# Performance work log

Hardware: AMD Instinct MI355X
Metric: run time of the kernel (lower is better)

Reference implementation:

```python
import jax, jax.numpy as jnp
import numpy as np

T = 8192
D_IN = 512
D_QK = 64
D_V = 64


def setup_inputs() -> dict:
    key = jax.random.key(0)
    kx, kq, kk, kv, kl = jax.random.split(key, 5)
    x = jax.random.normal(kx, (T, D_IN), dtype=jnp.float32)
    Wq = jax.random.normal(kq, (D_IN, D_QK), dtype=jnp.float32) * 0.02
    Wk = jax.random.normal(kk, (D_IN, D_QK), dtype=jnp.float32) * 0.02
    Wv = jax.random.normal(kv, (D_IN, D_V), dtype=jnp.float32) * 0.02
    l = jax.random.normal(kl, (T, T), dtype=jnp.float32) * 0.02
    return {"x": x, "Wq": Wq, "Wk": Wk, "Wv": Wv, "l": l}


def reference(x, Wq, Wk, Wv, l):
    # q: [T, d_qk], k: [T, d_qk], v: [T, d_v]
    q = x @ Wq
    k = x @ Wk
    v = x @ Wv
    # scores: [T, S] = (q k^T) elementwise-weighted by learned tril matrix
    scores = jnp.einsum("tn,sn->ts", q, k) * jnp.tril(l)
    # output: [T, d_v]
    return scores @ v
```

## Files before the change

### kernel.cpp

```cpp
#include <hip/hip_runtime.h>
#include <hip/hip_bf16.h>

#define TT 8192
#define DIN 512
#define DQK 64

typedef __attribute__((ext_vector_type(8))) short short8;
typedef __attribute__((ext_vector_type(4))) float f32x4;

__global__ __launch_bounds__(256) void init_kernel(
    const float* __restrict__ Wq, const float* __restrict__ Wk, const float* __restrict__ Wv,
    __hip_bfloat16* __restrict__ wtb, float* __restrict__ out, int n4)
{
    __shared__ float tile[64][65];
    const int b = blockIdx.x;
    const int tid = threadIdx.x;

    if (b >= 24) {
        const int nthr = 24 * 256;
        for (int i = (b - 24) * 256 + tid; i < n4; i += nthr)
            ((f32x4*)out)[i] = (f32x4){0.f, 0.f, 0.f, 0.f};
        return;
    }

    const int m = b >> 3;
    const float* W = m == 0 ? Wq : (m == 1 ? Wk : Wv);
    const int k0 = (b & 7) * 64;

    {
        const int col4 = (tid & 15) * 4;
        #pragma unroll
        for (int it = 0; it < 4; ++it) {
            const int row = (tid >> 4) + it * 16;
            float4 v = *(const float4*)&W[(size_t)(k0 + row) * DQK + col4];
            tile[row][col4 + 0] = v.x; tile[row][col4 + 1] = v.y;
            tile[row][col4 + 2] = v.z; tile[row][col4 + 3] = v.w;
        }
    }
    __syncthreads();
    {
        const int d = tid >> 2;
        const int kc = (tid & 3) * 16;
        short tmp[16];
        #pragma unroll
        for (int j = 0; j < 16; ++j) {
            __hip_bfloat16 h = __float2bfloat16(tile[kc + j][d]);
            tmp[j] = *(short*)&h;
        }
        short* dst = (short*)wtb + ((size_t)m * 64 + d) * DIN + k0 + kc;
        *(short8*)dst       = *(short8*)&tmp[0];
        *(short8*)(dst + 8) = *(short8*)&tmp[8];
    }
}

#define PP 72

__global__ __launch_bounds__(256) void proj_kernel(
    const float* __restrict__ x,
    const __hip_bfloat16* __restrict__ wtb,
    __hip_bfloat16* __restrict__ qb, __hip_bfloat16* __restrict__ kb,
    __hip_bfloat16* __restrict__ vt)
{
    __shared__ short xb[64][PP];
    __shared__ short wb[3][64][PP];

    const int rowBase = blockIdx.x * 64;
    const int tid = threadIdx.x;
    const int lane = tid & 63;
    const int w = tid >> 6;
    const int lo = lane & 15, hi = lane >> 4;

    f32x4 acc[3][4];
    #pragma unroll
    for (int m = 0; m < 3; ++m)
        #pragma unroll
        for (int cf = 0; cf < 4; ++cf) acc[m][cf] = (f32x4){0.f, 0.f, 0.f, 0.f};

    for (int kk = 0; kk < DIN; kk += 64) {
        {
            const int r = tid >> 2;
            const int c0 = (tid & 3) * 16;
            const float* xp = x + (size_t)(rowBase + r) * DIN + kk + c0;
            short tmp[16];
            #pragma unroll
            for (int j = 0; j < 16; j += 4) {
                float4 v = *(const float4*)(xp + j);
                __hip_bfloat16 h0 = __float2bfloat16(v.x);
                __hip_bfloat16 h1 = __float2bfloat16(v.y);
                __hip_bfloat16 h2 = __float2bfloat16(v.z);
                __hip_bfloat16 h3 = __float2bfloat16(v.w);
                tmp[j + 0] = *(short*)&h0; tmp[j + 1] = *(short*)&h1;
                tmp[j + 2] = *(short*)&h2; tmp[j + 3] = *(short*)&h3;
            }
            *(short8*)&xb[r][c0]     = *(short8*)&tmp[0];
            *(short8*)&xb[r][c0 + 8] = *(short8*)&tmp[8];
        }
        {
            const int d = tid >> 2;
            const int kc = (tid & 3) * 16;
            #pragma unroll
            for (int m = 0; m < 3; ++m) {
                const short* src = (const short*)wtb + ((size_t)m * 64 + d) * DIN + kk + kc;
                *(short8*)&wb[m][d][kc]     = *(const short8*)src;
                *(short8*)&wb[m][d][kc + 8] = *(const short8*)(src + 8);
            }
        }
        __syncthreads();

        short8 a0 = *(short8*)&xb[w * 16 + lo][hi * 8];
        short8 a1 = *(short8*)&xb[w * 16 + lo][32 + hi * 8];
        #pragma unroll
        for (int m = 0; m < 3; ++m) {
            #pragma unroll
            for (int cf = 0; cf < 4; ++cf) {
                short8 b0 = *(short8*)&wb[m][cf * 16 + lo][hi * 8];
                short8 b1 = *(short8*)&wb[m][cf * 16 + lo][32 + hi * 8];
                acc[m][cf] = __builtin_amdgcn_mfma_f32_16x16x32_bf16(a0, b0, acc[m][cf], 0, 0, 0);
                acc[m][cf] = __builtin_amdgcn_mfma_f32_16x16x32_bf16(a1, b1, acc[m][cf], 0, 0, 0);
            }
        }
        __syncthreads();
    }

    #pragma unroll
    for (int cf = 0; cf < 4; ++cf) {
        #pragma unroll
        for (int r = 0; r < 4; ++r) {
            const int tg = rowBase + w * 16 + hi * 4 + r;
            const int d  = cf * 16 + lo;
            __hip_bfloat16 hq = __float2bfloat16(acc[0][cf][r]);
            __hip_bfloat16 hk = __float2bfloat16(acc[1][cf][r]);
            __hip_bfloat16 hv = __float2bfloat16(acc[2][cf][r]);
            qb[(size_t)tg * DQK + d] = hq;
            kb[(size_t)tg * DQK + d] = hk;
            vt[(size_t)d * TT + tg]  = hv;
        }
    }
}

#define TM 128
#define TS 64
#define SCHUNK 512
#define LP 72

__global__ __launch_bounds__(512) void attn_kernel(
    const __hip_bfloat16* __restrict__ qb,
    const __hip_bfloat16* __restrict__ kb,
    const __hip_bfloat16* __restrict__ vt,
    const float* __restrict__ l,
    float* __restrict__ out)
{
    __shared__ short K_lds[TS][LP];
    __shared__ short V_lds[DQK][LP];
    __shared__ short S_lds[8][16][LP];

    const int bx = (gridDim.x - 1) - blockIdx.x;
    const int t0 = bx * TM;
    const int sStart = blockIdx.y * SCHUNK;
    if (sStart >= t0 + TM) return;
    const int sEnd = min(sStart + SCHUNK, t0 + TM);

    const int tid = threadIdx.x;
    const int lane = tid & 63;
    const int w = tid >> 6;
    const int lo = lane & 15, hi = lane >> 4;
    const int trow = t0 + w * 16;
    const int r0 = hi * 4;
    const bool waveActive = (sStart <= trow + 15);

    short8 qf0, qf1;
    {
        const short* qp = (const short*)qb + (size_t)(trow + lo) * DQK;
        qf0 = *(const short8*)(qp + hi * 8);
        qf1 = *(const short8*)(qp + 32 + hi * 8);
    }

    f32x4 acc_o[4];
    #pragma unroll
    for (int i = 0; i < 4; ++i) acc_o[i] = (f32x4){0.f, 0.f, 0.f, 0.f};

    float lvC[4][4];
    float lvN[4][4];
    if (waveActive) {
        #pragma unroll
        for (int sub = 0; sub < 4; ++sub) {
            const int s_glob = sStart + sub * 16 + lo;
            #pragma unroll
            for (int r = 0; r < 4; ++r) {
                const int tg = trow + r0 + r;
                lvC[sub][r] = (s_glob <= tg)
                    ? __builtin_nontemporal_load(&l[(size_t)tg * TT + s_glob]) : 0.f;
            }
        }
    }

    for (int s0 = sStart; s0 < sEnd; s0 += TS) {
        {
            const int row = tid >> 3;
            const int c8 = (tid & 7) * 8;
            *(short8*)&K_lds[row][c8] =
                *(const short8*)((const short*)kb + (size_t)(s0 + row) * DQK + c8);
            *(short8*)&V_lds[row][c8] =
                *(const short8*)((const short*)vt + (size_t)row * TT + s0 + c8);
        }
        __syncthreads();

        const bool active = (s0 <= trow + 15);
        const int sN = s0 + TS;
        const bool act_next = (sN < sEnd) && (sN <= trow + 15);

        if (act_next) {
            if (sN + 63 <= trow) {
                #pragma unroll
                for (int sub = 0; sub < 4; ++sub) {
                    const int s_glob = sN + sub * 16 + lo;
                    #pragma unroll
                    for (int r = 0; r < 4; ++r)
                        lvN[sub][r] = __builtin_nontemporal_load(
                            &l[(size_t)(trow + r0 + r) * TT + s_glob]);
                }
            } else {
                #pragma unroll
                for (int sub = 0; sub < 4; ++sub) {
                    const int s_glob = sN + sub * 16 + lo;
                    #pragma unroll
                    for (int r = 0; r < 4; ++r) {
                        const int tg = trow + r0 + r;
                        lvN[sub][r] = (s_glob <= tg)
                            ? __builtin_nontemporal_load(&l[(size_t)tg * TT + s_glob]) : 0.f;
                    }
                }
            }
        }

        if (active) {
            #pragma unroll
            for (int sub = 0; sub < 4; ++sub) {
                f32x4 acc = (f32x4){0.f, 0.f, 0.f, 0.f};
                short8 b0 = *(short8*)&K_lds[sub * 16 + lo][hi * 8];
                short8 b1 = *(short8*)&K_lds[sub * 16 + lo][32 + hi * 8];
                acc = __builtin_amdgcn_mfma_f32_16x16x32_bf16(qf0, b0, acc, 0, 0, 0);
                acc = __builtin_amdgcn_mfma_f32_16x16x32_bf16(qf1, b1, acc, 0, 0, 0);
                #pragma unroll
                for (int r = 0; r < 4; ++r) {
                    float sv = acc[r] * lvC[sub][r];
                    __hip_bfloat16 h = __float2bfloat16(sv);
                    S_lds[w][r0 + r][sub * 16 + lo] = *(short*)&h;
                }
            }
            short8 a0 = *(short8*)&S_lds[w][lo][hi * 8];
            short8 a1 = *(short8*)&S_lds[w][lo][32 + hi * 8];
            #pragma unroll
            for (int ds = 0; ds < 4; ++ds) {
                short8 b0 = *(short8*)&V_lds[ds * 16 + lo][hi * 8];
                short8 b1 = *(short8*)&V_lds[ds * 16 + lo][32 + hi * 8];
                acc_o[ds] = __builtin_amdgcn_mfma_f32_16x16x32_bf16(a0, b0, acc_o[ds], 0, 0, 0);
                acc_o[ds] = __builtin_amdgcn_mfma_f32_16x16x32_bf16(a1, b1, acc_o[ds], 0, 0, 0);
            }
        }
        __syncthreads();

        #pragma unroll
        for (int sub = 0; sub < 4; ++sub)
            #pragma unroll
            for (int r = 0; r < 4; ++r)
                lvC[sub][r] = lvN[sub][r];
    }

    if (waveActive) {
        #pragma unroll
        for (int ds = 0; ds < 4; ++ds) {
            #pragma unroll
            for (int r = 0; r < 4; ++r) {
                const int tg = trow + r0 + r;
                atomicAdd(&out[(size_t)tg * DQK + ds * 16 + lo], acc_o[ds][r]);
            }
        }
    }
}

extern "C" void kernel_launch(void* const* d_in, const int* in_sizes, int n_in,
                              void* d_out, int out_size, void* d_ws, size_t ws_size,
                              hipStream_t stream) {
    const float* x  = (const float*)d_in[0];
    const float* Wq = (const float*)d_in[1];
    const float* Wk = (const float*)d_in[2];
    const float* Wv = (const float*)d_in[3];
    const float* l  = (const float*)d_in[4];
    float* out = (float*)d_out;

    __hip_bfloat16* qb  = (__hip_bfloat16*)d_ws;
    __hip_bfloat16* kb  = qb + (size_t)TT * DQK;
    __hip_bfloat16* vt  = kb + (size_t)TT * DQK;
    __hip_bfloat16* wtb = vt + (size_t)TT * DQK;

    init_kernel<<<48, 256, 0, stream>>>(Wq, Wk, Wv, wtb, out, out_size / 4);
    proj_kernel<<<TT / 64, 256, 0, stream>>>(x, wtb, qb, kb, vt);
    attn_kernel<<<dim3(TT / TM, TT / SCHUNK), 512, 0, stream>>>(qb, kb, vt, l, out);
}
```

Before: 84.96 us.

## Transpose score MFMA to load l as float4 rows and pack S stores

```diff
diff --git a/kernel.cpp b/kernel.cpp
--- a/kernel.cpp
+++ b/kernel.cpp
@@ -7,6 +7,12 @@
 
 typedef __attribute__((ext_vector_type(8))) short short8;
 typedef __attribute__((ext_vector_type(4))) float f32x4;
+
+static __device__ __forceinline__ unsigned pack_bf16(float a, float b) {
+    __hip_bfloat16 ha = __float2bfloat16(a);
+    __hip_bfloat16 hb = __float2bfloat16(b);
+    return (unsigned)(*(unsigned short*)&ha) | ((unsigned)(*(unsigned short*)&hb) << 16);
+}
 
 __global__ __launch_bounds__(256) void init_kernel(
     const float* __restrict__ Wq, const float* __restrict__ Wk, const float* __restrict__ Wv,
@@ -140,7 +146,7 @@
 
 #define TM 128
 #define TS 64
-#define SCHUNK 512
+#define SCHUNK 256
 #define LP 72
 
 __global__ __launch_bounds__(512) void attn_kernel(
@@ -154,8 +160,7 @@
     __shared__ short V_lds[DQK][LP];
     __shared__ short S_lds[8][16][LP];
 
-    const int bx = (gridDim.x - 1) - blockIdx.x;
-    const int t0 = bx * TM;
+    const int t0 = blockIdx.x * TM;
     const int sStart = blockIdx.y * SCHUNK;
     if (sStart >= t0 + TM) return;
     const int sEnd = min(sStart + SCHUNK, t0 + TM);
@@ -165,12 +170,12 @@
     const int w = tid >> 6;
     const int lo = lane & 15, hi = lane >> 4;
     const int trow = t0 + w * 16;
-    const int r0 = hi * 4;
+    const int tmine = trow + lo;
     const bool waveActive = (sStart <= trow + 15);
 
     short8 qf0, qf1;
     {
-        const short* qp = (const short*)qb + (size_t)(trow + lo) * DQK;
+        const short* qp = (const short*)qb + (size_t)tmine * DQK;
         qf0 = *(const short8*)(qp + hi * 8);
         qf1 = *(const short8*)(qp + 32 + hi * 8);
     }
@@ -179,17 +184,22 @@
     #pragma unroll
     for (int i = 0; i < 4; ++i) acc_o[i] = (f32x4){0.f, 0.f, 0.f, 0.f};
 
-    float lvC[4][4];
-    float lvN[4][4];
+    const float* lrow = l + (size_t)tmine * TT;
+    const int sb = 4 * hi;
+
+    f32x4 lvC[4];
+    f32x4 lvN[4];
     if (waveActive) {
         #pragma unroll
         for (int sub = 0; sub < 4; ++sub) {
-            const int s_glob = sStart + sub * 16 + lo;
-            #pragma unroll
-            for (int r = 0; r < 4; ++r) {
-                const int tg = trow + r0 + r;
-                lvC[sub][r] = (s_glob <= tg)
-                    ? __builtin_nontemporal_load(&l[(size_t)tg * TT + s_glob]) : 0.f;
+            f32x4 raw = __builtin_nontemporal_load(
+                (const f32x4*)(lrow + sStart + sub * 16 + sb));
+            if (sStart + 63 <= trow) {
+                lvC[sub] = raw;
+            } else {
+                #pragma unroll
+                for (int r = 0; r < 4; ++r)
+                    lvC[sub][r] = (sStart + sub * 16 + sb + r <= tmine) ? raw[r] : 0.f;
             }
         }
     }
@@ -212,23 +222,17 @@
         if (act_next) {
             if (sN + 63 <= trow) {
                 #pragma unroll
-                for (int sub = 0; sub < 4; ++sub) {
-                    const int s_glob = sN + sub * 16 + lo;
-                    #pragma unroll
-                    for (int r = 0; r < 4; ++r)
-                        lvN[sub][r] = __builtin_nontemporal_load(
-                            &l[(size_t)(trow + r0 + r) * TT + s_glob]);
-                }
+                for (int sub = 0; sub < 4; ++sub)
+                    lvN[sub] = __builtin_nontemporal_load(
+                        (const f32x4*)(lrow + sN + sub * 16 + sb));
             } else {
                 #pragma unroll
                 for (int sub = 0; sub < 4; ++sub) {
-                    const int s_glob = sN + sub * 16 + lo;
+                    f32x4 raw = __builtin_nontemporal_load(
+                        (const f32x4*)(lrow + sN + sub * 16 + sb));
                     #pragma unroll
-                    for (int r = 0; r < 4; ++r) {
-                        const int tg = trow + r0 + r;
-                        lvN[sub][r] = (s_glob <= tg)
-                            ? __builtin_nontemporal_load(&l[(size_t)tg * TT + s_glob]) : 0.f;
-                    }
+                    for (int r = 0; r < 4; ++r)
+                        lvN[sub][r] = (sN + sub * 16 + sb + r <= tmine) ? raw[r] : 0.f;
                 }
             }
         }
@@ -239,14 +243,13 @@
                 f32x4 acc = (f32x4){0.f, 0.f, 0.f, 0.f};
                 short8 b0 = *(short8*)&K_lds[sub * 16 + lo][hi * 8];
                 short8 b1 = *(short8*)&K_lds[sub * 16 + lo][32 + hi * 8];
-                acc = __builtin_amdgcn_mfma_f32_16x16x32_bf16(qf0, b0, acc, 0, 0, 0);
-                acc = __builtin_amdgcn_mfma_f32_16x16x32_bf16(qf1, b1, acc, 0, 0, 0);
-                #pragma unroll
-                for (int r = 0; r < 4; ++r) {
-                    float sv = acc[r] * lvC[sub][r];
-                    __hip_bfloat16 h = __float2bfloat16(sv);
-                    S_lds[w][r0 + r][sub * 16 + lo] = *(short*)&h;
-                }
+                acc = __builtin_amdgcn_mfma_f32_16x16x32_bf16(b0, qf0, acc, 0, 0, 0);
+                acc = __builtin_amdgcn_mfma_f32_16x16x32_bf16(b1, qf1, acc, 0, 0, 0);
+                unsigned d0 = pack_bf16(acc[0] * lvC[sub][0], acc[1] * lvC[sub][1]);
+                unsigned d1 = pack_bf16(acc[2] * lvC[sub][2], acc[3] * lvC[sub][3]);
+                unsigned long long v = (unsigned long long)d0 |
+                                       ((unsigned long long)d1 << 32);
+                *(unsigned long long*)&S_lds[w][lo][sub * 16 + sb] = v;
             }
             short8 a0 = *(short8*)&S_lds[w][lo][hi * 8];
             short8 a1 = *(short8*)&S_lds[w][lo][32 + hi * 8];
@@ -262,9 +265,7 @@
 
         #pragma unroll
         for (int sub = 0; sub < 4; ++sub)
-            #pragma unroll
-            for (int r = 0; r < 4; ++r)
-                lvC[sub][r] = lvN[sub][r];
+            lvC[sub] = lvN[sub];
     }
 
     if (waveActive) {
@@ -272,7 +273,7 @@
         for (int ds = 0; ds < 4; ++ds) {
             #pragma unroll
             for (int r = 0; r < 4; ++r) {
-                const int tg = trow + r0 + r;
+                const int tg = trow + 4 * hi + r;
                 atomicAdd(&out[(size_t)tg * DQK + ds * 16 + lo], acc_o[ds][r]);
             }
         }
```

Measured after the change: 79.13 us. 1.07x faster.

## Split projection waves per matrix, halve attention S-chunk, drop reversed block order

Applied to the files above, without the earlier changes.

```diff
diff --git a/kernel.cpp b/kernel.cpp
--- a/kernel.cpp
+++ b/kernel.cpp
@@ -7,6 +7,16 @@
 
 typedef __attribute__((ext_vector_type(8))) short short8;
 typedef __attribute__((ext_vector_type(4))) float f32x4;
+
+static __device__ __forceinline__ short8 cvt8(const float* p) {
+    short tmp[8];
+    #pragma unroll
+    for (int j = 0; j < 8; ++j) {
+        __hip_bfloat16 h = __float2bfloat16(p[j]);
+        tmp[j] = *(short*)&h;
+    }
+    return *(short8*)tmp;
+}
 
 __global__ __launch_bounds__(256) void init_kernel(
     const float* __restrict__ Wq, const float* __restrict__ Wk, const float* __restrict__ Wv,
@@ -55,92 +65,83 @@
 
 #define PP 72
 
-__global__ __launch_bounds__(256) void proj_kernel(
+__global__ __launch_bounds__(384) void proj_kernel(
     const float* __restrict__ x,
     const __hip_bfloat16* __restrict__ wtb,
     __hip_bfloat16* __restrict__ qb, __hip_bfloat16* __restrict__ kb,
     __hip_bfloat16* __restrict__ vt)
 {
-    __shared__ short xb[64][PP];
+    __shared__ short xb[32][PP];
     __shared__ short wb[3][64][PP];
 
-    const int rowBase = blockIdx.x * 64;
+    const int rowBase = blockIdx.x * 32;
     const int tid = threadIdx.x;
     const int lane = tid & 63;
     const int w = tid >> 6;
+    const int m = w >> 1;
+    const int rh = w & 1;
     const int lo = lane & 15, hi = lane >> 4;
 
-    f32x4 acc[3][4];
+    f32x4 acc[4];
     #pragma unroll
-    for (int m = 0; m < 3; ++m)
-        #pragma unroll
-        for (int cf = 0; cf < 4; ++cf) acc[m][cf] = (f32x4){0.f, 0.f, 0.f, 0.f};
+    for (int cf = 0; cf < 4; ++cf) acc[cf] = (f32x4){0.f, 0.f, 0.f, 0.f};
 
     for (int kk = 0; kk < DIN; kk += 64) {
+        if (tid < 256) {
+            const int r = tid >> 3;
+            const int c0 = (tid & 7) * 8;
+            float xa[8];
+            *(float4*)&xa[0] = *(const float4*)(x + (size_t)(rowBase + r) * DIN + kk + c0);
+            *(float4*)&xa[4] = *(const float4*)(x + (size_t)(rowBase + r) * DIN + kk + c0 + 4);
+            *(short8*)&xb[r][c0] = cvt8(xa);
+        }
         {
-            const int r = tid >> 2;
-            const int c0 = (tid & 3) * 16;
-            const float* xp = x + (size_t)(rowBase + r) * DIN + kk + c0;
-            short tmp[16];
-            #pragma unroll
-            for (int j = 0; j < 16; j += 4) {
-                float4 v = *(const float4*)(xp + j);
-                __hip_bfloat16 h0 = __float2bfloat16(v.x);
-                __hip_bfloat16 h1 = __float2bfloat16(v.y);
-                __hip_bfloat16 h2 = __float2bfloat16(v.z);
-                __hip_bfloat16 h3 = __float2bfloat16(v.w);
-                tmp[j + 0] = *(short*)&h0; tmp[j + 1] = *(short*)&h1;
-                tmp[j + 2] = *(short*)&h2; tmp[j + 3] = *(short*)&h3;
-            }
-            *(short8*)&xb[r][c0]     = *(short8*)&tmp[0];
-            *(short8*)&xb[r][c0 + 8] = *(short8*)&tmp[8];
-        }
-        {
-            const int d = tid >> 2;
-            const int kc = (tid & 3) * 16;
-            #pragma unroll
-            for (int m = 0; m < 3; ++m) {
-                const short* src = (const short*)wtb + ((size_t)m * 64 + d) * DIN + kk + kc;
-                *(short8*)&wb[m][d][kc]     = *(const short8*)src;
-                *(short8*)&wb[m][d][kc + 8] = *(const short8*)(src + 8);
-            }
+            const int mm = tid / 128;
+            const int rem = tid & 127;
+            const int d = rem >> 1;
+            const int kc = (rem & 1) * 32;
+            const short* src = (const short*)wtb + ((size_t)mm * 64 + d) * DIN + kk + kc;
+            short* dst = &wb[mm][d][kc];
+            *(short8*)(dst + 0)  = *(const short8*)(src + 0);
+            *(short8*)(dst + 8)  = *(const short8*)(src + 8);
+            *(short8*)(dst + 16) = *(const short8*)(src + 16);
+            *(short8*)(dst + 24) = *(const short8*)(src + 24);
         }
         __syncthreads();
 
-        short8 a0 = *(short8*)&xb[w * 16 + lo][hi * 8];
-        short8 a1 = *(short8*)&xb[w * 16 + lo][32 + hi * 8];
-        #pragma unroll
-        for (int m = 0; m < 3; ++m) {
-            #pragma unroll
-            for (int cf = 0; cf < 4; ++cf) {
-                short8 b0 = *(short8*)&wb[m][cf * 16 + lo][hi * 8];
-                short8 b1 = *(short8*)&wb[m][cf * 16 + lo][32 + hi * 8];
-                acc[m][cf] = __builtin_amdgcn_mfma_f32_16x16x32_bf16(a0, b0, acc[m][cf], 0, 0, 0);
-                acc[m][cf] = __builtin_amdgcn_mfma_f32_16x16x32_bf16(a1, b1, acc[m][cf], 0, 0, 0);
-            }
+        short8 a0 = *(short8*)&xb[rh * 16 + lo][hi * 8];
+        short8 a1 = *(short8*)&xb[rh * 16 + lo][32 + hi * 8];
+        #pragma unroll
+        for (int cf = 0; cf < 4; ++cf) {
+            short8 b0 = *(short8*)&wb[m][cf * 16 + lo][hi * 8];
+            short8 b1 = *(short8*)&wb[m][cf * 16 + lo][32 + hi * 8];
+            acc[cf] = __builtin_amdgcn_mfma_f32_16x16x32_bf16(a0, b0, acc[cf], 0, 0, 0);
+            acc[cf] = __builtin_amdgcn_mfma_f32_16x16x32_bf16(a1, b1, acc[cf], 0, 0, 0);
         }
         __syncthreads();
     }
 
-    #pragma unroll
-    for (int cf = 0; cf < 4; ++cf) {
-        #pragma unroll
-        for (int r = 0; r < 4; ++r) {
-            const int tg = rowBase + w * 16 + hi * 4 + r;
-            const int d  = cf * 16 + lo;
-            __hip_bfloat16 hq = __float2bfloat16(acc[0][cf][r]);
-            __hip_bfloat16 hk = __float2bfloat16(acc[1][cf][r]);
-            __hip_bfloat16 hv = __float2bfloat16(acc[2][cf][r]);
-            qb[(size_t)tg * DQK + d] = hq;
-            kb[(size_t)tg * DQK + d] = hk;
-            vt[(size_t)d * TT + tg]  = hv;
-        }
+    if (m < 2) {
+        __hip_bfloat16* o = (m == 0) ? qb : kb;
+        #pragma unroll
+        for (int cf = 0; cf < 4; ++cf)
+            #pragma unroll
+            for (int r = 0; r < 4; ++r)
+                o[(size_t)(rowBase + rh * 16 + hi * 4 + r) * DQK + cf * 16 + lo] =
+                    __float2bfloat16(acc[cf][r]);
+    } else {
+        #pragma unroll
+        for (int cf = 0; cf < 4; ++cf)
+            #pragma unroll
+            for (int r = 0; r < 4; ++r)
+                vt[(size_t)(cf * 16 + lo) * TT + rowBase + rh * 16 + hi * 4 + r] =
+                    __float2bfloat16(acc[cf][r]);
     }
 }
 
 #define TM 128
 #define TS 64
-#define SCHUNK 512
+#define SCHUNK 256
 #define LP 72
 
 __global__ __launch_bounds__(512) void attn_kernel(
@@ -154,8 +155,7 @@
     __shared__ short V_lds[DQK][LP];
     __shared__ short S_lds[8][16][LP];
 
-    const int bx = (gridDim.x - 1) - blockIdx.x;
-    const int t0 = bx * TM;
+    const int t0 = blockIdx.x * TM;
     const int sStart = blockIdx.y * SCHUNK;
     if (sStart >= t0 + TM) return;
     const int sEnd = min(sStart + SCHUNK, t0 + TM);
@@ -295,6 +295,6 @@
     __hip_bfloat16* wtb = vt + (size_t)TT * DQK;
 
     init_kernel<<<48, 256, 0, stream>>>(Wq, Wk, Wv, wtb, out, out_size / 4);
-    proj_kernel<<<TT / 64, 256, 0, stream>>>(x, wtb, qb, kb, vt);
+    proj_kernel<<<TT / 32, 384, 0, stream>>>(x, wtb, qb, kb, vt);
     attn_kernel<<<dim3(TT / TM, TT / SCHUNK), 512, 0, stream>>>(qb, kb, vt, l, out);
 }
```

New measurement: 80.67 us. 5.1% less time.
